# Performance work log

Measured on AMD Instinct MI355X. Metric: run time of the kernel, lower is better.

Reference implementation:

```python
import jax, jax.numpy as jnp
import numpy as np

IMAGE_SIZE = 256
DET = int(IMAGE_SIZE * 2 ** 0.5 + 0.5)  # 362 detector bins (diagonal coverage)
US = 4
N_ACQ = 45                     # acquired views: 0,4,...,176 degrees
N_FULL = (N_ACQ - 1) * US + 1  # 177 full (upsampled) views


def setup_inputs() -> dict:
    key = jax.random.key(0)
    k1, k2 = jax.random.split(key)
    x_source = jax.random.normal(k1, (2, 1, IMAGE_SIZE, IMAGE_SIZE), jnp.float32)
    s_target = jax.random.normal(k2, (2, 1, DET, N_ACQ), jnp.float32)
    theta_acq = np.arange(0, 180, 4, dtype=np.float64)  # 45 acquired angles
    segs = [np.linspace(theta_acq[i], theta_acq[i + 1], US + 1)[:-1] for i in range(N_ACQ - 1)]
    theta_full = np.concatenate(segs + [theta_acq[-1:]]).astype(np.float32)  # [177]
    acq_idx = (np.arange(N_ACQ) * US).astype(np.int32)  # positions of acquired angles in theta_full
    return {"x_source": x_source, "s_target": s_target,
            "thetas_deg": jnp.asarray(theta_full), "acq_idx": jnp.asarray(acq_idx)}


def bilinear_gather(img, xs, ys):
    # img: [B,C,H,W]; xs, ys: pixel coords [A,det,det]; zero outside the image.
    H, W = img.shape[-2], img.shape[-1]
    x0 = jnp.floor(xs); y0 = jnp.floor(ys)
    wx = xs - x0; wy = ys - y0
    x0i = x0.astype(jnp.int32); y0i = y0.astype(jnp.int32)

    def get(yi, xi):
        valid = (xi >= 0) & (xi < W) & (yi >= 0) & (yi < H)
        v = img[:, :, jnp.clip(yi, 0, H - 1), jnp.clip(xi, 0, W - 1)]  # [B,C,A,det,det]
        return jnp.where(valid, v, 0.0)

    return (get(y0i, x0i) * (1 - wy) * (1 - wx)
            + get(y0i, x0i + 1) * (1 - wy) * wx
            + get(y0i + 1, x0i) * wy * (1 - wx)
            + get(y0i + 1, x0i + 1) * wy * wx)


def radon(x, thetas_rad, det):
    # Ray-sum projection: sino[theta, t] = sum_s image(t*cos - s*sin, t*sin + s*cos)
    B, C, H, W = x.shape
    t = jnp.arange(det, dtype=x.dtype) - (det - 1) / 2.0  # centered detector/ray coord
    cos = jnp.cos(thetas_rad)[:, None, None]
    sin = jnp.sin(thetas_rad)[:, None, None]
    T = t[None, :, None]; S = t[None, None, :]
    xs = T * cos - S * sin + (W - 1) / 2.0  # [A,det,det]
    ys = T * sin + S * cos + (H - 1) / 2.0
    return bilinear_gather(x, xs, ys).sum(-1)  # [B,C,A,det]


def ramp_filter(size):
    # skimage/pytorch_radon style ramp built from its real-space kernel
    n = np.concatenate([np.arange(1, size // 2 + 1, 2), np.arange(size // 2 - 1, 0, -2)])
    f = np.zeros(size)
    f[0] = 0.25
    f[1::2] = -1.0 / (np.pi * n) ** 2
    return jnp.asarray(2 * np.real(np.fft.fft(f)), dtype=jnp.float32)


def fbp(sino, thetas_rad, image_size):
    # Filtered back-projection. sino: [B,C,det,A]
    B, C, det, A = sino.shape
    pad = max(64, int(2 ** np.ceil(np.log2(2 * det))))
    filt = ramp_filter(pad)  # [pad]
    sp = jnp.pad(sino, ((0, 0), (0, 0), (0, pad - det), (0, 0)))
    sf = jnp.fft.ifft(jnp.fft.fft(sp, axis=2) * filt[None, None, :, None], axis=2).real
    sf = jnp.transpose(sf[:, :, :det, :], (0, 1, 3, 2)).astype(sino.dtype)  # [B,C,A,det]
    g = jnp.arange(image_size, dtype=sino.dtype) - (image_size - 1) / 2.0
    cos = jnp.cos(thetas_rad); sin = jnp.sin(thetas_rad)
    # detector coordinate hit by each pixel, per angle: t = x*cos + y*sin
    t = (cos[:, None, None] * g[None, None, :]
         + sin[:, None, None] * g[None, :, None] + (det - 1) / 2.0)  # [A,H,W]
    t = t.reshape(A, -1)
    t0 = jnp.floor(t)
    w = t - t0
    t0i = t0.astype(jnp.int32)
    aidx = jnp.arange(A)[:, None]

    def samp(ti):
        valid = (ti >= 0) & (ti < det)
        return jnp.where(valid, sf[:, :, aidx, jnp.clip(ti, 0, det - 1)], 0.0)  # [B,C,A,HW]

    v = samp(t0i) * (1 - w) + samp(t0i + 1) * w
    reco = v.sum(2) * (jnp.pi / (2 * A))
    return reco.reshape(B, C, image_size, image_size)


def reference(x_source, s_target, thetas_deg, acq_idx):
    th = thetas_deg * (jnp.pi / 180.0)
    s = radon(x_source, th, DET)          # [B,C,A,det]
    s = jnp.transpose(s, (0, 1, 3, 2))    # [B,C,det,A] -- angle axis last, as in the module
    # masked data-consistency update: acquired columns become (target - predicted)
    s = s.at[..., acq_idx].set(s_target - s[..., acq_idx])
    return fbp(s, th, IMAGE_SIZE)
```

## Files before the change

### kernel.cpp

```cpp
#include <hip/hip_runtime.h>
#include <math.h>

#define IMG   256
#define NFULL 177
#define DETN  362
#define NACQ  45
#define PAD   1024

#define SINO_OFF 0
#define SF_OFF   131072

#define TTILE  32
#define HALF_T 180.5f
#define TILE_N 5112

__constant__ const int kByOrder[12] = {5, 6, 4, 7, 3, 8, 2, 9, 1, 10, 0, 11};

__device__ __forceinline__ void gload16(const float* g, float* l) {
    __builtin_amdgcn_global_load_lds(
        (const __attribute__((address_space(1))) void*)g,
        (__attribute__((address_space(3))) void*)l, 16, 0, 0);
}

template<int P, int L>
__device__ __forceinline__ float radon_core(
    const float* __restrict__ img,
    float* tile,
    const float c, const float s,
    const float xbase, const float ybase,
    const float xAB_mn, const float yAB_mn, const float yAB_mx,
    const int SloB, const int ShiB, const int tid)
{
    constexpr int W4   = P / 4;
    constexpr int HMAX = TILE_N / P;
    const int ts   = tid & 7;
    const int wid  = tid >> 6;
    const int lane = tid & 63;
    float val = 0.0f;

    for (int Sseg = SloB; Sseg < ShiB; Sseg += L) {
        const float sv0 = (float)Sseg - HALF_T;
        const float sv1 = sv0 + (float)(L - 1);
        const float xmn = xAB_mn - sv1 * s;
        const float ya  = sv0 * c, yb = sv1 * c;
        const float ymn = yAB_mn + fminf(ya, yb);
        const float ymx = yAB_mx + fmaxf(ya, yb);
        const int ix0  = (int)floorf(xmn) - 1;
        const int iy0  = (int)floorf(ymn) - 1;
        const int ix0a = ix0 & ~3;
        const int h    = min((int)floorf(ymx) + 3 - iy0, HMAX);
        const int total4 = W4 * h;

        const bool interior = (ix0a >= 0) & (iy0 >= 0) &
                              (ix0a + P <= IMG) & (iy0 + h <= IMG);
        if (interior) {
            const float* __restrict__ src = img + iy0 * IMG + ix0a;
            for (int f0 = wid * 64; f0 < total4; f0 += 256) {
                const int f = f0 + lane;
                if (f < total4) {
                    const int r  = f / W4;
                    const int c4 = f - r * W4;
                    gload16(src + r * IMG + (c4 << 2), tile + (f0 << 2));
                }
            }
        } else {
            for (int f = tid; f < total4; f += 256) {
                const int r  = f / W4;
                const int c4 = f - r * W4;
                const int gy = iy0 + r;
                const int gx = ix0a + (c4 << 2);
                const bool ok = ((unsigned)gy < (unsigned)IMG) &
                                ((unsigned)gx <= (unsigned)(IMG - 4));
                float4 v = make_float4(0.f, 0.f, 0.f, 0.f);
                if (ok) v = *(const float4*)(img + gy * IMG + gx);
                *(float4*)(tile + (f << 2)) = v;
            }
        }
        __syncthreads();

        const float xoff = xbase - (float)ix0a;
        const float yoff = ybase - (float)iy0;
        const int Send = min(Sseg + L, ShiB);

        auto samp = [&](float sval) {
            const float xs  = fmaf(-sval, s, xoff);
            const float ys  = fmaf(sval, c, yoff);
            const float x0f = floorf(xs);
            const float y0f = floorf(ys);
            const float wx  = xs - x0f;
            const float wy  = ys - y0f;
            const int base = (int)fmaf(y0f, (float)P, x0f);
            const float v00 = tile[base];
            const float v01 = tile[base + 1];
            const float v10 = tile[base + P];
            const float v11 = tile[base + P + 1];
            const float h0 = fmaf(wx, v01 - v00, v00);
            const float h1 = fmaf(wx, v11 - v10, v10);
            val += fmaf(wy, h1 - h0, h0);
        };

        if (Send - Sseg == L) {
            const float s0 = (float)(Sseg + ts) - HALF_T;
            #pragma unroll 4
            for (int u = 0; u < L / 8; ++u) samp(s0 + (float)(8 * u));
        } else {
            for (int S = Sseg + ts; S < Send; S += 8) samp((float)S - HALF_T);
        }
        __syncthreads();
    }
    return val;
}

__global__ __launch_bounds__(256, 8) void radon_kernel(
    const float* __restrict__ x,
    const float* __restrict__ thetas,
    float* __restrict__ sino)
{
    const int blk = blockIdx.x;
    const int b = blk / NFULL;
    const int a = blk - b * NFULL;
    const int T0 = kByOrder[blockIdx.y] * TTILE;
    const int tid = threadIdx.x;
    const int ts = tid & 7;
    const int tt = tid >> 3;
    const int T = T0 + tt;

    __shared__ __align__(16) float tile[TILE_N];
    __shared__ int sRange[2];
    __shared__ int sSel;

    const float th = thetas[a] * (float)(M_PI / 180.0);
    const float c = cosf(th);
    const float s = sinf(th);
    const float cx = (IMG - 1) * 0.5f;
    const float cy = (IMG - 1) * 0.5f;
    const float Tc = (float)T - HALF_T;
    const float xbase = Tc * c + cx;
    const float ybase = Tc * s + cy;

    float lo = -1e30f, hi = 1e30f;
    bool empty = (T >= DETN);
    {   const float aa = -s;
        if (aa > 1e-5f)       { lo = fmaxf(lo, (-1.0f - xbase) / aa); hi = fminf(hi, (256.0f - xbase) / aa); }
        else if (aa < -1e-5f) { lo = fmaxf(lo, (256.0f - xbase) / aa); hi = fminf(hi, (-1.0f - xbase) / aa); }
        else if (xbase <= -1.0f || xbase >= 256.0f) empty = true;
    }
    {   const float aa = c;
        if (aa > 1e-5f)       { lo = fmaxf(lo, (-1.0f - ybase) / aa); hi = fminf(hi, (256.0f - ybase) / aa); }
        else if (aa < -1e-5f) { lo = fmaxf(lo, (256.0f - ybase) / aa); hi = fminf(hi, (-1.0f - ybase) / aa); }
        else if (ybase <= -1.0f || ybase >= 256.0f) empty = true;
    }
    lo = fmaxf(lo, -200.0f);
    hi = fminf(hi, 200.0f);
    int Slo = max(0, (int)floorf(lo + HALF_T) - 1);
    int Shi = min(DETN, (int)floorf(hi + HALF_T) + 2);
    if (empty || Shi < Slo) { Slo = 0; Shi = 0; }

    if (tid == 0) { sRange[0] = DETN; sRange[1] = 0; }
    __syncthreads();
    if (Shi > Slo) { atomicMin(&sRange[0], Slo); atomicMax(&sRange[1], Shi); }

    if (tid < 64) {
        const int ltt = tid >> 3, lts = tid & 7;
        const float ac = fabsf(c), as = fabsf(s);
        const float spx = 31.f * ac + 63.f * as;
        const float spy = 31.f * as + 63.f * ac;
        const int hm[3] = {75, 71, 67};
        int best = 5, bcost = 1 << 30;
        #pragma unroll
        for (int p = 0; p < 3; ++p) {
            const float Pf = 68.f + 4.f * (float)p;
            const float dT = s * Pf + c;
            const float dS = c * Pf - s;
            const int bank = (int)floorf((float)ltt * dT + (float)lts * dS + 0.5f) & 31;
            unsigned long long m = ~0ull;
            #pragma unroll
            for (int bit = 0; bit < 5; ++bit) {
                const unsigned long long bb = __ballot((bank >> bit) & 1);
                m &= ((bank >> bit) & 1) ? bb : ~bb;
            }
            int cnt = __popcll(m);
            #pragma unroll
            for (int d = 1; d < 64; d <<= 1) cnt = max(cnt, __shfl_xor(cnt, d, 64));
            if (spx <= Pf - 8.05f && spy <= (float)hm[p] - 5.05f) {
                if (2 * cnt < bcost) { bcost = 2 * cnt; best = p; }
            }
            if (2 * cnt + 3 < bcost) { bcost = 2 * cnt + 3; best = p + 3; }
        }
        if (tid == 0) sSel = best;
    }
    __syncthreads();
    const int SloB = sRange[0], ShiB = sRange[1];
    const int selv = sSel;

    const float TcA = (float)T0 - HALF_T;
    const float TcB = (float)(T0 + TTILE - 1) - HALF_T;
    const float xAB_mn = fminf(TcA * c + cx, TcB * c + cx);
    const float yAB_mn = fminf(TcA * s + cy, TcB * s + cy);
    const float yAB_mx = fmaxf(TcA * s + cy, TcB * s + cy);

    const float* __restrict__ img = x + b * IMG * IMG;

    float val;
    switch (selv) {
    case 0:  val = radon_core<68,64>(img, tile, c, s, xbase, ybase,
                                     xAB_mn, yAB_mn, yAB_mx, SloB, ShiB, tid); break;
    case 1:  val = radon_core<72,64>(img, tile, c, s, xbase, ybase,
                                     xAB_mn, yAB_mn, yAB_mx, SloB, ShiB, tid); break;
    case 2:  val = radon_core<76,64>(img, tile, c, s, xbase, ybase,
                                     xAB_mn, yAB_mn, yAB_mx, SloB, ShiB, tid); break;
    case 3:  val = radon_core<68,48>(img, tile, c, s, xbase, ybase,
                                     xAB_mn, yAB_mn, yAB_mx, SloB, ShiB, tid); break;
    case 4:  val = radon_core<72,48>(img, tile, c, s, xbase, ybase,
                                     xAB_mn, yAB_mn, yAB_mx, SloB, ShiB, tid); break;
    default: val = radon_core<76,48>(img, tile, c, s, xbase, ybase,
                                     xAB_mn, yAB_mn, yAB_mx, SloB, ShiB, tid); break;
    }

    val += __shfl_xor(val, 1, 8);
    val += __shfl_xor(val, 2, 8);
    val += __shfl_xor(val, 4, 8);
    if (ts == 0 && T < DETN) {
        sino[(b * NFULL + a) * DETN + T] = val;
    }
}

__global__ __launch_bounds__(192) void dc_filter_kernel(
    const float* __restrict__ sino,
    const float* __restrict__ st,
    const int*   __restrict__ acq,
    float* __restrict__ sf)
{
    const int blk = blockIdx.x;
    const int b = blk / NFULL;
    const int a = blk - b * NFULL;
    const int tid = threadIdx.x;

    __shared__ float col[DETN];
    __shared__ float gf[PAD];

    const float SC = (float)(M_PI / (2.0 * NFULL));
    const float c0 = 0.5f * SC;
    for (int n = tid; n < PAD; n += 192) {
        float v = 0.0f;
        if (n & 1) {
            const int d = (n < PAD - n) ? n : (PAD - n);
            const float pd = (float)M_PI * (float)d;
            v = -2.0f / (pd * pd) * SC;
        }
        gf[n] = v;
    }

    int inv = -1;
    for (int i = 0; i < NACQ; ++i) {
        if (acq[i] == a) inv = i;
    }

    for (int m = tid; m < DETN; m += 192) {
        float val = sino[(b * NFULL + a) * DETN + m];
        if (inv >= 0) {
            val = st[(b * DETN + m) * NACQ + inv] - val;
        }
        col[m] = val;
    }
    __syncthreads();

    const int T = blockIdx.y * 181 + tid;
    if (tid < 181) {
        const int m0 = (T + 1) & 1;
        float acc = c0 * col[T];
        #pragma unroll 4
        for (int k = 0; k < 181; ++k) {
            const int m = m0 + 2 * k;
            acc += col[m] * gf[(T - m) & (PAD - 1)];
        }
        sf[(b * NFULL + a) * DETN + T] = acc;
    }
}

__global__ __launch_bounds__(256) void backproject_kernel(
    const float* __restrict__ sf,
    const float* __restrict__ thetas,
    float* __restrict__ out)
{
    __shared__ float cb[2 * NFULL];
    __shared__ float red[256];
    const int tid = threadIdx.x;
    const int lane  = tid & 63;
    const int phase = tid >> 6;
    const int pix = blockIdx.x * 64 + lane;
    const int b = pix >> 16;
    const int y = (pix >> 8) & 255;
    const int xq = pix & 255;
    const float gx = (float)xq - (IMG - 1) * 0.5f;
    const float gy = (float)y  - (IMG - 1) * 0.5f;

    for (int a = tid; a < NFULL; a += 256) {
        float th = thetas[a] * (float)(M_PI / 180.0);
        cb[2 * a]     = cosf(th);
        cb[2 * a + 1] = fmaf(sinf(th), gy, HALF_T);
    }
    __syncthreads();

    const float* __restrict__ sfb = sf + b * NFULL * DETN;

    float acc = 0.0f;
    #pragma unroll 4
    for (int a = phase; a < NFULL; a += 4) {
        const float cs = cb[2 * a];
        const float bs = cb[2 * a + 1];
        const float t = fmaf(cs, gx, bs);
        const float t0f = floorf(t);
        const float w = t - t0f;
        const float* row = sfb + a * DETN + (int)t0f;
        const float v0 = row[0];
        const float v1 = row[1];
        acc += v0 + w * (v1 - v0);
    }
    red[tid] = acc;
    __syncthreads();
    if (tid < 64) {
        out[blockIdx.x * 64 + tid] =
            red[tid] + red[tid + 64] + red[tid + 128] + red[tid + 192];
    }
}

extern "C" void kernel_launch(void* const* d_in, const int* in_sizes, int n_in,
                              void* d_out, int out_size, void* d_ws, size_t ws_size,
                              hipStream_t stream) {
    const float* x      = (const float*)d_in[0];
    const float* st     = (const float*)d_in[1];
    const float* thetas = (const float*)d_in[2];
    const int*   acq    = (const int*)d_in[3];
    float* out  = (float*)d_out;
    float* wsf  = (float*)d_ws;
    float* sino = wsf + SINO_OFF;
    float* sf   = wsf + SF_OFF;

    dim3 gA(2 * NFULL, 12);
    radon_kernel<<<gA, 256, 0, stream>>>(x, thetas, sino);
    dim3 gB(2 * NFULL, 2);
    dc_filter_kernel<<<gB, 192, 0, stream>>>(sino, st, acq, sf);
    backproject_kernel<<<(2 * IMG * IMG) / 64, 256, 0, stream>>>(sf, thetas, out);
}
```

Baseline: 126.1 us.

## Double-buffer radon image tiles with smaller 32-step segments

Replaces the single shared-memory tile, which was loaded and then consumed with a barrier between each segment of ray steps, with two half-size buffers. The window for the next 32-step segment is prefetched into the alternate buffer while the current one is sampled, so global-to-LDS loads overlap with the bilinear sampling. Segment length drops from 48/64 to 32, tile pitches shrink to 44-60, and the pitch selection heuristic is reworked to match. The cost is more segment iterations and barriers, plus a partially-filled last wavefront of async loads.

```diff
diff --git a/kernel.cpp b/kernel.cpp
--- a/kernel.cpp
+++ b/kernel.cpp
@@ -12,7 +12,8 @@
 
 #define TTILE  32
 #define HALF_T 180.5f
-#define TILE_N 5112
+#define SEGL   32
+#define TILE_SEG 2548
 
 __constant__ const int kByOrder[12] = {5, 6, 4, 7, 3, 8, 2, 9, 1, 10, 0, 11};
 
@@ -22,7 +23,7 @@
         (__attribute__((address_space(3))) void*)l, 16, 0, 0);
 }
 
-template<int P, int L>
+template<int P>
 __device__ __forceinline__ float radon_core(
     const float* __restrict__ img,
     float* tile,
@@ -32,15 +33,14 @@
     const int SloB, const int ShiB, const int tid)
 {
     constexpr int W4   = P / 4;
-    constexpr int HMAX = TILE_N / P;
+    constexpr int HMAX = TILE_SEG / P;
     const int ts   = tid & 7;
     const int wid  = tid >> 6;
     const int lane = tid & 63;
-    float val = 0.0f;
-
-    for (int Sseg = SloB; Sseg < ShiB; Sseg += L) {
+
+    auto window = [&](int Sseg) -> int4 {
         const float sv0 = (float)Sseg - HALF_T;
-        const float sv1 = sv0 + (float)(L - 1);
+        const float sv1 = sv0 + (float)(SEGL - 1);
         const float xmn = xAB_mn - sv1 * s;
         const float ya  = sv0 * c, yb = sv1 * c;
         const float ymn = yAB_mn + fminf(ya, yb);
@@ -49,38 +49,63 @@
         const int iy0  = (int)floorf(ymn) - 1;
         const int ix0a = ix0 & ~3;
         const int h    = min((int)floorf(ymx) + 3 - iy0, HMAX);
-        const int total4 = W4 * h;
-
-        const bool interior = (ix0a >= 0) & (iy0 >= 0) &
-                              (ix0a + P <= IMG) & (iy0 + h <= IMG);
-        if (interior) {
-            const float* __restrict__ src = img + iy0 * IMG + ix0a;
-            for (int f0 = wid * 64; f0 < total4; f0 += 256) {
-                const int f = f0 + lane;
-                if (f < total4) {
-                    const int r  = f / W4;
-                    const int c4 = f - r * W4;
-                    gload16(src + r * IMG + (c4 << 2), tile + (f0 << 2));
-                }
+        const int inter = (ix0a >= 0) & (iy0 >= 0) &
+                          (ix0a + P <= IMG) & (iy0 + h <= IMG);
+        return make_int4(ix0a, iy0, h, inter);
+    };
+
+    auto stage = [&](const int4 wp, float* tb) {
+        const int total4 = W4 * wp.z;
+        const int nfull  = total4 & ~63;
+        if (wp.w) {
+            const float* __restrict__ src = img + wp.y * IMG + wp.x;
+            for (int f0 = wid * 64; f0 < nfull; f0 += 256) {
+                const int f  = f0 + lane;
+                const int r  = f / W4;
+                const int c4 = f - r * W4;
+                gload16(src + r * IMG + (c4 << 2), tb + (f0 << 2));
+            }
+            const int f = nfull + tid;
+            if (f < total4) {
+                const int r  = f / W4;
+                const int c4 = f - r * W4;
+                gload16(src + r * IMG + (c4 << 2), tb + (nfull << 2));
             }
         } else {
             for (int f = tid; f < total4; f += 256) {
                 const int r  = f / W4;
                 const int c4 = f - r * W4;
-                const int gy = iy0 + r;
-                const int gx = ix0a + (c4 << 2);
+                const int gy = wp.y + r;
+                const int gx = wp.x + (c4 << 2);
                 const bool ok = ((unsigned)gy < (unsigned)IMG) &
                                 ((unsigned)gx <= (unsigned)(IMG - 4));
                 float4 v = make_float4(0.f, 0.f, 0.f, 0.f);
                 if (ok) v = *(const float4*)(img + gy * IMG + gx);
-                *(float4*)(tile + (f << 2)) = v;
+                *(float4*)(tb + (f << 2)) = v;
             }
         }
-        __syncthreads();
-
-        const float xoff = xbase - (float)ix0a;
-        const float yoff = ybase - (float)iy0;
-        const int Send = min(Sseg + L, ShiB);
+    };
+
+    float val = 0.0f;
+    if (SloB >= ShiB) return val;
+
+    int4 wp = window(SloB);
+    stage(wp, tile);
+    __syncthreads();
+
+    int cur = 0;
+    for (int Sseg = SloB; Sseg < ShiB; Sseg += SEGL) {
+        const int Snext = Sseg + SEGL;
+        int4 wpn = wp;
+        if (Snext < ShiB) {
+            wpn = window(Snext);
+            stage(wpn, tile + (cur ^ 1) * TILE_SEG);
+        }
+
+        const float* __restrict__ tb = tile + cur * TILE_SEG;
+        const float xoff = xbase - (float)wp.x;
+        const float yoff = ybase - (float)wp.y;
+        const int Send = min(Snext, ShiB);
 
         auto samp = [&](float sval) {
             const float xs  = fmaf(-sval, s, xoff);
@@ -90,23 +115,25 @@
             const float wx  = xs - x0f;
             const float wy  = ys - y0f;
             const int base = (int)fmaf(y0f, (float)P, x0f);
-            const float v00 = tile[base];
-            const float v01 = tile[base + 1];
-            const float v10 = tile[base + P];
-            const float v11 = tile[base + P + 1];
+            const float v00 = tb[base];
+            const float v01 = tb[base + 1];
+            const float v10 = tb[base + P];
+            const float v11 = tb[base + P + 1];
             const float h0 = fmaf(wx, v01 - v00, v00);
             const float h1 = fmaf(wx, v11 - v10, v10);
             val += fmaf(wy, h1 - h0, h0);
         };
 
-        if (Send - Sseg == L) {
+        if (Send - Sseg == SEGL) {
             const float s0 = (float)(Sseg + ts) - HALF_T;
-            #pragma unroll 4
-            for (int u = 0; u < L / 8; ++u) samp(s0 + (float)(8 * u));
+            #pragma unroll
+            for (int u = 0; u < SEGL / 8; ++u) samp(s0 + (float)(8 * u));
         } else {
             for (int S = Sseg + ts; S < Send; S += 8) samp((float)S - HALF_T);
         }
         __syncthreads();
+        wp = wpn;
+        cur ^= 1;
     }
     return val;
 }
@@ -125,7 +152,7 @@
     const int tt = tid >> 3;
     const int T = T0 + tt;
 
-    __shared__ __align__(16) float tile[TILE_N];
+    __shared__ __align__(16) float tile[2 * TILE_SEG];
     __shared__ int sRange[2];
     __shared__ int sSel;
 
@@ -163,13 +190,12 @@
     if (tid < 64) {
         const int ltt = tid >> 3, lts = tid & 7;
         const float ac = fabsf(c), as = fabsf(s);
-        const float spx = 31.f * ac + 63.f * as;
-        const float spy = 31.f * as + 63.f * ac;
-        const int hm[3] = {75, 71, 67};
-        int best = 5, bcost = 1 << 30;
+        const float span = 31.f * (ac + as);
+        const int hm[5] = {57, 53, 49, 45, 42};
+        int best = 2, bcost = 1 << 30;
         #pragma unroll
-        for (int p = 0; p < 3; ++p) {
-            const float Pf = 68.f + 4.f * (float)p;
+        for (int p = 0; p < 5; ++p) {
+            const float Pf = 44.f + 4.f * (float)p;
             const float dT = s * Pf + c;
             const float dS = c * Pf - s;
             const int bank = (int)floorf((float)ltt * dT + (float)lts * dS + 0.5f) & 31;
@@ -182,10 +208,8 @@
             int cnt = __popcll(m);
             #pragma unroll
             for (int d = 1; d < 64; d <<= 1) cnt = max(cnt, __shfl_xor(cnt, d, 64));
-            if (spx <= Pf - 8.05f && spy <= (float)hm[p] - 5.05f) {
-                if (2 * cnt < bcost) { bcost = 2 * cnt; best = p; }
-            }
-            if (2 * cnt + 3 < bcost) { bcost = 2 * cnt + 3; best = p + 3; }
+            const bool fit = (span <= Pf - 8.05f) && (span <= (float)hm[p] - 5.05f);
+            if (fit && cnt < bcost) { bcost = cnt; best = p; }
         }
         if (tid == 0) sSel = best;
     }
@@ -203,18 +227,16 @@
 
     float val;
     switch (selv) {
-    case 0:  val = radon_core<68,64>(img, tile, c, s, xbase, ybase,
-                                     xAB_mn, yAB_mn, yAB_mx, SloB, ShiB, tid); break;
-    case 1:  val = radon_core<72,64>(img, tile, c, s, xbase, ybase,
-                                     xAB_mn, yAB_mn, yAB_mx, SloB, ShiB, tid); break;
-    case 2:  val = radon_core<76,64>(img, tile, c, s, xbase, ybase,
-                                     xAB_mn, yAB_mn, yAB_mx, SloB, ShiB, tid); break;
-    case 3:  val = radon_core<68,48>(img, tile, c, s, xbase, ybase,
-                                     xAB_mn, yAB_mn, yAB_mx, SloB, ShiB, tid); break;
-    case 4:  val = radon_core<72,48>(img, tile, c, s, xbase, ybase,
-                                     xAB_mn, yAB_mn, yAB_mx, SloB, ShiB, tid); break;
-    default: val = radon_core<76,48>(img, tile, c, s, xbase, ybase,
-                                     xAB_mn, yAB_mn, yAB_mx, SloB, ShiB, tid); break;
+    case 0:  val = radon_core<44>(img, tile, c, s, xbase, ybase,
+                                  xAB_mn, yAB_mn, yAB_mx, SloB, ShiB, tid); break;
+    case 1:  val = radon_core<48>(img, tile, c, s, xbase, ybase,
+                                  xAB_mn, yAB_mn, yAB_mx, SloB, ShiB, tid); break;
+    case 2:  val = radon_core<52>(img, tile, c, s, xbase, ybase,
+                                  xAB_mn, yAB_mn, yAB_mx, SloB, ShiB, tid); break;
+    case 3:  val = radon_core<56>(img, tile, c, s, xbase, ybase,
+                                  xAB_mn, yAB_mn, yAB_mx, SloB, ShiB, tid); break;
+    default: val = radon_core<60>(img, tile, c, s, xbase, ybase,
+                                  xAB_mn, yAB_mn, yAB_mx, SloB, ShiB, tid); break;
     }
 
     val += __shfl_xor(val, 1, 8);
```

New measurement: 126.8 us. Within noise of the previous version (+0.6%).
